# Performance work log

Hardware: AMD Instinct MI355X
Metric: run time of the kernel (lower is better)

## Reference

```python
import jax, jax.numpy as jnp
import numpy as np

EPS = 1e-6
B, T, J, D, H = 8, 512, 26, 256, 8
DH = D // H
HID = 4 * D


def logmap0(x):
    # x: [..., d+1] on hyperboloid (curvature -1). Tangent at origin -> [..., d]
    x0 = jnp.clip(x[..., :1], 1.0 + 1e-7, None)
    xs = x[..., 1:]
    n = jnp.maximum(jnp.linalg.norm(xs, axis=-1, keepdims=True), EPS)
    return jnp.arccosh(x0) * xs / n


def expmap0(v):
    # v: [..., d] tangent at origin -> [..., d+1] on hyperboloid
    n = jnp.maximum(jnp.linalg.norm(v, axis=-1, keepdims=True), EPS)
    return jnp.concatenate([jnp.cosh(n), jnp.sinh(n) * v / n], axis=-1)


def layernorm(v, g, b):
    m = jnp.mean(v, axis=-1, keepdims=True)
    var = jnp.var(v, axis=-1, keepdims=True)
    return (v - m) * jax.lax.rsqrt(var + 1e-5) * g + b


def lorentz_residual(x, z):
    # Lorentz centroid: normalize x+z so <m,m>_L = -1
    m = x + z
    mink = -m[..., :1] ** 2 + jnp.sum(m[..., 1:] ** 2, axis=-1, keepdims=True)
    return m / jnp.sqrt(jnp.clip(-mink, EPS, None))


def setup_inputs() -> dict:
    key = jax.random.key(0)
    ks = jax.random.split(key, 12)
    xs = jax.random.normal(ks[0], (B, T, J, D), jnp.float32) * 0.5
    x0 = jnp.sqrt(1.0 + jnp.sum(xs ** 2, axis=-1, keepdims=True))
    x = jnp.concatenate([x0, xs], axis=-1)  # valid points on H^d
    s = 1.0 / np.sqrt(D)
    inp = {
        "x": x,
        "g1": jnp.ones((D,), jnp.float32), "beta1": jnp.zeros((D,), jnp.float32),
        "Wq": jax.random.normal(ks[1], (D, D), jnp.float32) * s,
        "Wk": jax.random.normal(ks[2], (D, D), jnp.float32) * s,
        "Wv": jax.random.normal(ks[3], (D, D), jnp.float32) * s,
        "Wo": jax.random.normal(ks[4], (D, D), jnp.float32) * s,
        "bq": jnp.zeros((D,), jnp.float32), "bk": jnp.zeros((D,), jnp.float32),
        "bv": jnp.zeros((D,), jnp.float32), "bo": jnp.zeros((D,), jnp.float32),
        "g2": jnp.ones((D,), jnp.float32), "beta2": jnp.zeros((D,), jnp.float32),
        "W1": jax.random.normal(ks[5], (D, HID), jnp.float32) * s,
        "bf1": jnp.zeros((HID,), jnp.float32),
        "W2": jax.random.normal(ks[6], (HID, D), jnp.float32) * (1.0 / np.sqrt(HID)),
        "bf2": jnp.zeros((D,), jnp.float32),
    }
    return inp


def reference(x, g1, beta1, Wq, Wk, Wv, Wo, bq, bk, bv, bo, g2, beta2, W1, bf1, W2, bf2):
    # norm1: tangent-space LayerNorm
    u = layernorm(logmap0(x), g1, beta1)            # [B,T,J,D]
    xn = expmap0(u)
    # linear temporal attention (per joint, across T)
    t = logmap0(xn)
    q = (t @ Wq + bq).reshape(B, T, J, H, DH)
    k = (t @ Wk + bk).reshape(B, T, J, H, DH)
    v = (t @ Wv + bv).reshape(B, T, J, H, DH)
    pq = jax.nn.elu(q) + 1.0
    pk = jax.nn.elu(k) + 1.0
    kv = jnp.einsum('btjhk,btjhd->bjhkd', pk, v)    # O(T) global context
    ksum = jnp.sum(pk, axis=1)                      # [B,J,H,DH]
    num = jnp.einsum('btjhk,bjhkd->btjhd', pq, kv)
    den = jnp.einsum('btjhk,bjhk->btjh', pq, ksum)[..., None] + EPS
    o = (num / den).reshape(B, T, J, D) @ Wo + bo
    z = expmap0(o)
    # Lorentz (Minkowski) residual
    h = lorentz_residual(x, z)
    # norm2 + FFN in tangent space
    u2 = layernorm(logmap0(h), g2, beta2)
    f = jax.nn.gelu(u2 @ W1 + bf1) @ W2 + bf2
    return expmap0(f)
```

## Files before the change

### kernel.cpp

```cpp
#include <hip/hip_runtime.h>
#include <hip/hip_bf16.h>
#include <math.h>


#define EPSF 1e-6f
#define B_ 8
#define T_ 512
#define J_ 26
#define D_ 256
#define H_ 8
#define DH_ 32
#define HID_ 1024
#define NP1 257
#define R_ (B_*T_*J_)
#define NBJ (B_*J_)
#define NBH (NBJ*H_)

typedef float  f32x4  __attribute__((ext_vector_type(4)));
typedef short  s16x8  __attribute__((ext_vector_type(8)));
typedef short  s16x4  __attribute__((ext_vector_type(4)));

__device__ __forceinline__ int rp_to_r(int rp) {
  int bj = rp >> 9, t = rp & 511;
  int b = bj / 26, j = bj - 26 * b;
  return (b * 512 + t) * 26 + j;
}

__device__ __forceinline__ void async16(const void* g, void* l) {
  __builtin_amdgcn_global_load_lds(
      (const __attribute__((address_space(1))) unsigned int*)g,
      (__attribute__((address_space(3))) unsigned int*)l, 16, 0, 0);
}

__device__ __forceinline__ float wave_sum(float v) {
#pragma unroll
  for (int m = 32; m; m >>= 1) v += __shfl_xor(v, m, 64);
  return v;
}

__global__ __launch_bounds__(256) void k_wconv(const float* __restrict__ W,
                                               __hip_bfloat16* __restrict__ Wt,
                                               int K, int N) {
  __shared__ float tile[32][33];
  int n0 = blockIdx.x * 32, k0 = blockIdx.y * 32;
  int tx = threadIdx.x, ty = threadIdx.y;
#pragma unroll
  for (int i = ty; i < 32; i += 8) tile[i][tx] = W[(size_t)(k0 + i) * N + n0 + tx];
  __syncthreads();
#pragma unroll
  for (int i = ty; i < 32; i += 8)
    Wt[(size_t)(n0 + i) * K + k0 + tx] = __float2bfloat16(tile[tx][i]);
}

__global__ __launch_bounds__(256) void k_t(const float* __restrict__ x,
                                           const float* __restrict__ g1,
                                           const float* __restrict__ beta1,
                                           __hip_bfloat16* __restrict__ t) {
  int rp = blockIdx.x * 4 + (threadIdx.x >> 6);
  int l = threadIdx.x & 63;
  int r = rp_to_r(rp);
  const float* xr = x + (size_t)r * NP1;
  float xs[4];
#pragma unroll
  for (int i = 0; i < 4; ++i) xs[i] = xr[1 + l + 64*i];
  float p1 = xs[0]+xs[1]+xs[2]+xs[3];
  float p2 = xs[0]*xs[0]+xs[1]*xs[1]+xs[2]*xs[2]+xs[3]*xs[3];
  float s1 = wave_sum(p1);
  float s2 = wave_sum(p2);
  float mean = s1 * (1.0f/256.0f);
  float var = s2 * (1.0f/256.0f) - mean*mean;
  float rstd = rsqrtf(var + 1e-5f);
#pragma unroll
  for (int i = 0; i < 4; ++i) {
    int c = l + 64*i;
    t[(size_t)rp * D_ + c] = __float2bfloat16((xs[i]-mean)*rstd*g1[c] + beta1[c]);
  }
}

#define PHASE(BUF, MH, NH, GIDX, DO_VM) {                                      \
    s16x8 af_[4][2]; s16x8 bf_[2][2];                                          \
    const char* ab_ = lds + ((BUF)*2+(MH))*16384;                              \
    const char* bb_ = lds + 65536 + ((BUF)*2+(NH))*16384;                      \
    _Pragma("unroll") for (int f_ = 0; f_ < 4; ++f_)                           \
      _Pragma("unroll") for (int ks_ = 0; ks_ < 2; ++ks_)                      \
        af_[f_][ks_] = *(const s16x8*)(ab_ + aoffs[f_][ks_]);                  \
    _Pragma("unroll") for (int ni_ = 0; ni_ < 2; ++ni_)                        \
      _Pragma("unroll") for (int ks_ = 0; ks_ < 2; ++ks_)                      \
        bf_[ni_][ks_] = *(const s16x8*)(bb_ + boffs[ni_][ks_]);                \
    STAGE_HALF((GIDX) + 6);                                                    \
    if (DO_VM) asm volatile("s_waitcnt vmcnt(4)" ::: "memory");                \
    asm volatile("s_barrier" ::: "memory");                                    \
    __builtin_amdgcn_sched_barrier(0);                                         \
    __builtin_amdgcn_s_setprio(1);                                             \
    _Pragma("unroll") for (int ks_ = 0; ks_ < 2; ++ks_)                        \
      _Pragma("unroll") for (int f_ = 0; f_ < 4; ++f_)                         \
        _Pragma("unroll") for (int ni_ = 0; ni_ < 2; ++ni_)                    \
          acc[(MH)*4+f_][(NH)*2+ni_] = __builtin_amdgcn_mfma_f32_16x16x32_bf16(\
              bf_[ni_][ks_], af_[f_][ks_], acc[(MH)*4+f_][(NH)*2+ni_], 0,0,0); \
    __builtin_amdgcn_s_setprio(0);                                             \
    asm volatile("s_barrier" ::: "memory");                                    \
  }

template<int ACT, int EPI, int KDIM>
__global__ __launch_bounds__(512, 2) void k_gemm(const __hip_bfloat16* __restrict__ A,
                                                 const __hip_bfloat16* __restrict__ Bt,
                                                 const float* __restrict__ bias,
                                                 void* __restrict__ Cout,
                                                 int M, int N, int mOff) {
  extern __shared__ char lds[];
  constexpr int NKT = KDIM / 64;
  int tid = threadIdx.x;
  int w = tid >> 6, l = tid & 63;
  int wr = w >> 2, wc = w & 3;
  int ml = l & 15, quad = l >> 4;
  int n0 = blockIdx.x * 256, m0 = blockIdx.y * 256;

  const short* Ag = (const short*)A + (size_t)m0 * KDIM;
  const short* Bg = (const short*)Bt + (size_t)n0 * KDIM;

  int srow = w*8 + (l >> 3);
  int scol = (((l & 7) ^ ((l >> 3) & 7)) * 8);

  auto STAGE_HALF = [&](int n) {
    if (n >= 4*NKT) return;
    int kt = n >> 2;
    int isB = n & 1, h = (n >> 1) & 1, buf = kt & 1;
    const short* src = isB ? Bg : Ag;
    const short* g0 = src + (size_t)(h*128 + srow) * KDIM + kt*64 + scol;
    char* dst = lds + isB*65536 + (buf*2 + h)*16384 + w*1024;
    async16(g0, dst);
    async16(g0 + (size_t)64 * KDIM, dst + 8192);
  };

  int aoffs[4][2], boffs[2][2];
#pragma unroll
  for (int f = 0; f < 4; ++f) {
    int r = wr*64 + f*16 + ml;
#pragma unroll
    for (int ks = 0; ks < 2; ++ks)
      aoffs[f][ks] = (r*128 + ks*64 + quad*16) ^ ((ml & 7) << 4);
  }
#pragma unroll
  for (int ni = 0; ni < 2; ++ni) {
    int rb = wc*32 + ni*16 + ml;
#pragma unroll
    for (int ks = 0; ks < 2; ++ks)
      boffs[ni][ks] = (rb*128 + ks*64 + quad*16) ^ ((ml & 7) << 4);
  }

  f32x4 acc[8][4];
#pragma unroll
  for (int i = 0; i < 8; ++i)
#pragma unroll
    for (int j = 0; j < 4; ++j) acc[i][j] = {0.f, 0.f, 0.f, 0.f};

#pragma unroll
  for (int n = 0; n < 6; ++n) STAGE_HALF(n);
  asm volatile("s_waitcnt vmcnt(4)" ::: "memory");
  asm volatile("s_barrier" ::: "memory");

  for (int cc = 0; cc < NKT/2; ++cc) {
    int g0 = cc * 8;
    PHASE(0, 0, 0, g0+0, 0)
    PHASE(0, 0, 1, g0+1, 0)
    PHASE(0, 1, 0, g0+2, 0)
    PHASE(0, 1, 1, g0+3, 1)
    PHASE(1, 0, 0, g0+4, 0)
    PHASE(1, 0, 1, g0+5, 0)
    PHASE(1, 1, 0, g0+6, 0)
    PHASE(1, 1, 1, g0+7, 1)
  }

  if (EPI == 0) {
#pragma unroll
    for (int mi = 0; mi < 8; ++mi) {
      size_t row = (size_t)(m0 + (mi>>2)*128 + wr*64 + (mi&3)*16 + ml);
#pragma unroll
      for (int nj = 0; nj < 4; ++nj) {
        int col = n0 + (nj>>1)*128 + wc*32 + (nj&1)*16 + quad*4;
        f32x4 bj = *(const f32x4*)&bias[col];
        f32x4 v = acc[mi][nj] + bj;
        if (ACT == 1) {
#pragma unroll
          for (int e = 0; e < 4; ++e) v[e] = (v[e] > 0.0f) ? v[e] + 1.0f : __expf(v[e]);
        } else if (ACT == 2) {
#pragma unroll
          for (int e = 0; e < 4; ++e) {
            float vv = v[e], v2 = vv * vv;
            float ex = __expf(vv * fmaf(v2, -0.0713548327f, -1.5957691216f));
            v[e] = vv * __builtin_amdgcn_rcpf(1.0f + ex);
          }
        }
        s16x4 sv;
#pragma unroll
        for (int e = 0; e < 4; ++e) {
          __hip_bfloat16 b = __float2bfloat16(v[e]);
          sv[e] = *(short*)&b;
        }
        *(s16x4*)&((__hip_bfloat16*)Cout)[row * N + col] = sv;
      }
    }
  } else {
    float* out = (float*)Cout;
    float* red = (float*)lds;
    f32x4 bj4[4];
#pragma unroll
    for (int nj = 0; nj < 4; ++nj)
      bj4[nj] = *(const f32x4*)&bias[(nj>>1)*128 + wc*32 + (nj&1)*16 + quad*4];
    float n2[8];
#pragma unroll
    for (int mi = 0; mi < 8; ++mi) {
      float p = 0.f;
#pragma unroll
      for (int nj = 0; nj < 4; ++nj)
#pragma unroll
        for (int e = 0; e < 4; ++e) {
          float f = acc[mi][nj][e] + bj4[nj][e];
          p = fmaf(f, f, p);
        }
      p += __shfl_xor(p, 16, 64);
      p += __shfl_xor(p, 32, 64);
      n2[mi] = p;
    }
    __syncthreads();
    if (quad == 0) {
#pragma unroll
      for (int mi = 0; mi < 8; ++mi)
        red[((wr*4 + wc)*8 + mi)*16 + ml] = n2[mi];
    }
    __syncthreads();
#pragma unroll
    for (int mi = 0; mi < 8; ++mi) {
      float s = 0.f;
#pragma unroll
      for (int w2 = 0; w2 < 4; ++w2)
        s += red[((wr*4 + w2)*8 + mi)*16 + ml];
      n2[mi] = s;
    }
#pragma unroll
    for (int mi = 0; mi < 8; ++mi) {
      int rowp = m0 + (mi>>2)*128 + wr*64 + (mi&3)*16 + ml;
      int r = rp_to_r(mOff + rowp);
      float* orow = out + (size_t)r * NP1;
      float n = fmaxf(sqrtf(n2[mi]), EPSF);
      float e = __expf(n);
      float ie = 1.0f / e;
      float sc = (e - ie) * 0.5f / n;
      if (wc == 0 && quad == 0) orow[0] = (e + ie) * 0.5f;
#pragma unroll
      for (int nj = 0; nj < 4; ++nj) {
        int col = (nj>>1)*128 + wc*32 + (nj&1)*16 + quad*4;
#pragma unroll
        for (int e2 = 0; e2 < 4; ++e2)
          orow[1 + col + e2] = sc * (acc[mi][nj][e2] + bj4[nj][e2]);
      }
    }
  }
}

__global__ __launch_bounds__(256) void k_kv(const __hip_bfloat16* __restrict__ pk,
                                            const __hip_bfloat16* __restrict__ v,
                                            float* __restrict__ kv,
                                            float* __restrict__ ksum) {
  __shared__ float spk[32][32];
  __shared__ float sv [32][32];
  int blk = blockIdx.x;
  int h = blk & 7, bj = blk >> 3;
  int tid = threadIdx.x;
  int row = tid >> 3, cg = tid & 7;
  int k0 = tid >> 5, dd = tid & 31;

  const short* pkg = (const short*)pk + (size_t)bj*512*256 + h*32 + cg*4;
  const short* vg  = (const short*)v  + (size_t)bj*512*256 + h*32 + cg*4;

  s16x4 rp_, rv_;
  auto GLOAD = [&](int c) {
    size_t off = (size_t)(c*32 + row) * 256;
    rp_ = *(const s16x4*)(pkg + off);
    rv_ = *(const s16x4*)(vg + off);
  };

  float acc[4] = {0.f, 0.f, 0.f, 0.f};
  float ks = 0.f;

  GLOAD(0);
  for (int c = 0; c < 16; ++c) {
    f32x4 pf, vf;
#pragma unroll
    for (int e = 0; e < 4; ++e) {
      pf[e] = __uint_as_float(((unsigned)(unsigned short)rp_[e]) << 16);
      vf[e] = __uint_as_float(((unsigned)(unsigned short)rv_[e]) << 16);
    }
    *(f32x4*)&spk[row][cg*4] = pf;
    *(f32x4*)&sv [row][cg*4] = vf;
    __syncthreads();
    if (c < 15) GLOAD(c + 1);
#pragma unroll
    for (int q = 0; q < 32; ++q) {
      float vv = sv[q][dd];
#pragma unroll
      for (int m = 0; m < 4; ++m) acc[m] = fmaf(spk[q][k0 + 8*m], vv, acc[m]);
    }
    if (tid < 32) {
#pragma unroll
      for (int q = 0; q < 32; ++q) ks += spk[q][tid];
    }
    __syncthreads();
  }

  float* kvp = kv + (size_t)blk * 1024;
#pragma unroll
  for (int m = 0; m < 4; ++m) kvp[(k0 + 8*m)*32 + dd] = acc[m];
  if (tid < 32) ksum[(size_t)blk * 32 + tid] = ks;
}

__global__ __launch_bounds__(256) void k_attn(const __hip_bfloat16* __restrict__ pq,
                                              const float* __restrict__ kv,
                                              const float* __restrict__ ksum,
                                              __hip_bfloat16* __restrict__ attn) {
  __shared__ float psf[32][264];
  __shared__ float dens[32][8];
  int bj = blockIdx.y;
  int t0 = blockIdx.x * 32;
  int g0 = bj * 512 + t0;
  int tid = threadIdx.x, w = tid >> 6, l = tid & 63;
  int h = w*2 + (l >> 5), dd = l & 31;

  const float* kvp = kv + ((size_t)bj * 8 + h) * (DH_*DH_);
  float kvreg[32];
#pragma unroll
  for (int k = 0; k < 32; ++k) kvreg[k] = kvp[k*32 + dd];

  for (int tr = 0; tr < 32; ++tr)
    psf[tr][tid] = __bfloat162float(pq[(size_t)(g0 + tr) * D_ + tid]);
  __syncthreads();

  {
    int tr = tid & 31, hh = tid >> 5;
    const float* ksp = ksum + ((size_t)bj * 8 + hh) * DH_;
    float dsum = 0.f;
#pragma unroll
    for (int k = 0; k < 32; ++k) dsum = fmaf(psf[tr][hh*32 + k], ksp[k], dsum);
    dens[tr][hh] = dsum;
  }
  __syncthreads();

  for (int tr = 0; tr < 32; ++tr) {
    const float* pr = &psf[tr][h*32];
    float num = 0.f;
#pragma unroll
    for (int k = 0; k < 32; ++k) num = fmaf(pr[k], kvreg[k], num);
    float rden = __builtin_amdgcn_rcpf(dens[tr][h] + EPSF);
    attn[(size_t)(g0 + tr) * D_ + tid] = __float2bfloat16(num * rden);
  }
}

__global__ __launch_bounds__(256) void k_u2(const __hip_bfloat16* __restrict__ o,
                                            const float* __restrict__ x,
                                            const float* __restrict__ g2,
                                            const float* __restrict__ beta2,
                                            __hip_bfloat16* __restrict__ u2) {
  int rp = blockIdx.x * 4 + (threadIdx.x >> 6);
  int l = threadIdx.x & 63;
  int r = rp_to_r(rp);
  const float* xr = x + (size_t)r * NP1;
  float ov[4], xs[4];
#pragma unroll
  for (int i = 0; i < 4; ++i) {
    ov[i] = __bfloat162float(o[(size_t)rp * D_ + l + 64*i]);
    xs[i] = xr[1 + l + 64*i];
  }
  float p2 = ov[0]*ov[0]+ov[1]*ov[1]+ov[2]*ov[2]+ov[3]*ov[3];
  float s2o = wave_sum(p2);
  float no = fmaxf(sqrtf(s2o), EPSF);
  float e = __expf(no);
  float c = (e - 1.0f/e) * 0.5f / no;
  float mi[4];
#pragma unroll
  for (int i = 0; i < 4; ++i) mi[i] = xs[i] + c * ov[i];
  float q1 = mi[0]+mi[1]+mi[2]+mi[3];
  float q2 = mi[0]*mi[0]+mi[1]*mi[1]+mi[2]*mi[2]+mi[3]*mi[3];
  float s1 = wave_sum(q1);
  float s2 = wave_sum(q2);
  float mean = s1 * (1.0f/256.0f);
  float var = s2 * (1.0f/256.0f) - mean*mean;
  float rstd = rsqrtf(var + 1e-5f);
#pragma unroll
  for (int i = 0; i < 4; ++i) {
    int cc = l + 64*i;
    u2[(size_t)rp * D_ + cc] = __float2bfloat16((mi[i]-mean)*rstd*g2[cc] + beta2[cc]);
  }
}

extern "C" void kernel_launch(void* const* d_in, const int* in_sizes, int n_in,
                              void* d_out, int out_size, void* d_ws, size_t ws_size,
                              hipStream_t stream) {
  const float* x     = (const float*)d_in[0];
  const float* g1    = (const float*)d_in[1];
  const float* beta1 = (const float*)d_in[2];
  const float* Wq    = (const float*)d_in[3];
  const float* Wk    = (const float*)d_in[4];
  const float* Wv    = (const float*)d_in[5];
  const float* Wo    = (const float*)d_in[6];
  const float* bq    = (const float*)d_in[7];
  const float* bk    = (const float*)d_in[8];
  const float* bv    = (const float*)d_in[9];
  const float* bo    = (const float*)d_in[10];
  const float* g2    = (const float*)d_in[11];
  const float* beta2 = (const float*)d_in[12];
  const float* W1    = (const float*)d_in[13];
  const float* bf1   = (const float*)d_in[14];
  const float* W2    = (const float*)d_in[15];
  const float* bf2   = (const float*)d_in[16];
  float* out = (float*)d_out;
  char* ws = (char*)d_ws;

  size_t off = 0;
  __hip_bfloat16* wqT = (__hip_bfloat16*)(ws + off); off += (size_t)D_*D_*2;
  __hip_bfloat16* wkT = (__hip_bfloat16*)(ws + off); off += (size_t)D_*D_*2;
  __hip_bfloat16* wvT = (__hip_bfloat16*)(ws + off); off += (size_t)D_*D_*2;
  __hip_bfloat16* woT = (__hip_bfloat16*)(ws + off); off += (size_t)D_*D_*2;
  __hip_bfloat16* w1T = (__hip_bfloat16*)(ws + off); off += (size_t)HID_*D_*2;
  __hip_bfloat16* w2T = (__hip_bfloat16*)(ws + off); off += (size_t)D_*HID_*2;
  float* kvb = (float*)(ws + off); off += (size_t)NBH*(DH_*DH_)*4;
  float* ksb = (float*)(ws + off); off += (size_t)NBH*DH_*4;
  off = (off + 255) & ~(size_t)255;
  __hip_bfloat16* tb = (__hip_bfloat16*)(ws + off); off += (size_t)R_*D_*2;
  __hip_bfloat16* qb = (__hip_bfloat16*)(ws + off); off += (size_t)R_*D_*2;
  __hip_bfloat16* kb = (__hip_bfloat16*)(ws + off); off += (size_t)R_*D_*2;
  __hip_bfloat16* vb = (__hip_bfloat16*)(ws + off); off += (size_t)R_*D_*2;
  __hip_bfloat16* hid = (__hip_bfloat16*)(ws + off); off += (size_t)(R_/2)*HID_*2;

  static bool attr_done = false;
  if (!attr_done) {
    hipFuncSetAttribute((const void*)k_gemm<1,0,256>,  hipFuncAttributeMaxDynamicSharedMemorySize, 131072);
    hipFuncSetAttribute((const void*)k_gemm<0,0,256>,  hipFuncAttributeMaxDynamicSharedMemorySize, 131072);
    hipFuncSetAttribute((const void*)k_gemm<2,0,256>,  hipFuncAttributeMaxDynamicSharedMemorySize, 131072);
    hipFuncSetAttribute((const void*)k_gemm<0,2,1024>, hipFuncAttributeMaxDynamicSharedMemorySize, 131072);
    attr_done = true;
  }

  dim3 tconv(32, 8);
  k_wconv<<<dim3(D_/32,  D_/32),  tconv, 0, stream>>>(Wq, wqT, D_,  D_);
  k_wconv<<<dim3(D_/32,  D_/32),  tconv, 0, stream>>>(Wk, wkT, D_,  D_);
  k_wconv<<<dim3(D_/32,  D_/32),  tconv, 0, stream>>>(Wv, wvT, D_,  D_);
  k_wconv<<<dim3(D_/32,  D_/32),  tconv, 0, stream>>>(Wo, woT, D_,  D_);
  k_wconv<<<dim3(HID_/32, D_/32), tconv, 0, stream>>>(W1, w1T, D_,  HID_);
  k_wconv<<<dim3(D_/32, HID_/32), tconv, 0, stream>>>(W2, w2T, HID_, D_);

  k_t<<<R_/4, 256, 0, stream>>>(x, g1, beta1, tb);

  dim3 gqkv(D_/256, R_/256);
  k_gemm<1,0,256><<<gqkv, 512, 131072, stream>>>(tb, wqT, bq, qb, R_, D_, 0);
  k_gemm<1,0,256><<<gqkv, 512, 131072, stream>>>(tb, wkT, bk, kb, R_, D_, 0);
  k_gemm<0,0,256><<<gqkv, 512, 131072, stream>>>(tb, wvT, bv, vb, R_, D_, 0);

  k_kv<<<NBH, 256, 0, stream>>>(kb, vb, kvb, ksb);
  k_attn<<<dim3(T_/32, NBJ), 256, 0, stream>>>(qb, kvb, ksb, kb);

  k_gemm<0,0,256><<<gqkv, 512, 131072, stream>>>(kb, woT, bo, vb, R_, D_, 0);
  k_u2<<<R_/4, 256, 0, stream>>>(vb, x, g2, beta2, tb);

  const int Rc = R_ / 2;
  for (int c = 0; c < 2; ++c) {
    k_gemm<2,0,256><<<dim3(HID_/256, Rc/256), 512, 131072, stream>>>(
        tb + (size_t)c * Rc * D_, w1T, bf1, hid, Rc, HID_, 0);
    k_gemm<0,2,1024><<<dim3(1, Rc/256), 512, 131072, stream>>>(
        hid, w2T, bf2, out, Rc, D_, c * Rc);
  }
}
```

Before: 782.2 us.

## Fuse Q/K/V projections into one GEMM launch and register-tile kv reduction

The three separate Q, K and V projection GEMMs become one launch with three column blocks. Each block picks its bias and activation (ELU+1 for Q and K, none for V) from its column index and writes to the matching output buffer. This relies on the transposed weights and the output buffers sitting next to each other in the workspace. The k_kv kernel now gives each thread a 4x4 outer-product tile built from vectorised LDS reads on padded rows, with the time chunk split across warps and a final cross-warp reduction through shared memory. This aims to cut launch and scheduling overhead and LDS traffic, at the cost of an extra reduction step and barrier.

```diff
diff --git a/kernel.cpp b/kernel.cpp
--- a/kernel.cpp
+++ b/kernel.cpp
@@ -105,6 +105,8 @@
 __global__ __launch_bounds__(512, 2) void k_gemm(const __hip_bfloat16* __restrict__ A,
                                                  const __hip_bfloat16* __restrict__ Bt,
                                                  const float* __restrict__ bias,
+                                                 const float* __restrict__ bias2,
+                                                 const float* __restrict__ bias3,
                                                  void* __restrict__ Cout,
                                                  int M, int N, int mOff) {
   extern __shared__ char lds[];
@@ -171,19 +173,24 @@
     PHASE(1, 1, 1, g0+7, 1)
   }
 
-  if (EPI == 0) {
+  if (EPI == 0 || EPI == 1) {
+    int bi = n0 >> 8;
+    const float* bsel = (EPI == 1) ? (bi == 0 ? bias : bi == 1 ? bias2 : bias3)
+                                   : bias;
+    int doElu = (EPI == 1) ? (bi < 2) : (ACT == 1);
 #pragma unroll
     for (int mi = 0; mi < 8; ++mi) {
       size_t row = (size_t)(m0 + (mi>>2)*128 + wr*64 + (mi&3)*16 + ml);
 #pragma unroll
       for (int nj = 0; nj < 4; ++nj) {
         int col = n0 + (nj>>1)*128 + wc*32 + (nj&1)*16 + quad*4;
-        f32x4 bj = *(const f32x4*)&bias[col];
+        int colL = col & 255;
+        f32x4 bj = *(const f32x4*)&bsel[(EPI == 1) ? colL : col];
         f32x4 v = acc[mi][nj] + bj;
-        if (ACT == 1) {
+        if (doElu) {
 #pragma unroll
           for (int e = 0; e < 4; ++e) v[e] = (v[e] > 0.0f) ? v[e] + 1.0f : __expf(v[e]);
-        } else if (ACT == 2) {
+        } else if (EPI == 0 && ACT == 2) {
 #pragma unroll
           for (int e = 0; e < 4; ++e) {
             float vv = v[e], v2 = vv * vv;
@@ -197,7 +204,12 @@
           __hip_bfloat16 b = __float2bfloat16(v[e]);
           sv[e] = *(short*)&b;
         }
-        *(s16x4*)&((__hip_bfloat16*)Cout)[row * N + col] = sv;
+        if (EPI == 1) {
+          short* cb = (short*)Cout + (size_t)bi * R_ * 256;
+          *(s16x4*)&cb[row * 256 + colL] = sv;
+        } else {
+          *(s16x4*)&((__hip_bfloat16*)Cout)[row * N + col] = sv;
+        }
       }
     }
   } else {
@@ -262,13 +274,17 @@
                                             const __hip_bfloat16* __restrict__ v,
                                             float* __restrict__ kv,
                                             float* __restrict__ ksum) {
-  __shared__ float spk[32][32];
-  __shared__ float sv [32][32];
+  __shared__ float sbuf[4096];
+  __shared__ float sks[4][32];
   int blk = blockIdx.x;
   int h = blk & 7, bj = blk >> 3;
   int tid = threadIdx.x;
+  int w = tid >> 6, l = tid & 63;
   int row = tid >> 3, cg = tid & 7;
-  int k0 = tid >> 5, dd = tid & 31;
+  int kg = l >> 3, dg = l & 7;
+
+  float* spk = sbuf;
+  float* sv  = sbuf + 1152;
 
   const short* pkg = (const short*)pk + (size_t)bj*512*256 + h*32 + cg*4;
   const short* vg  = (const short*)v  + (size_t)bj*512*256 + h*32 + cg*4;
@@ -280,8 +296,8 @@
     rv_ = *(const s16x4*)(vg + off);
   };
 
-  float acc[4] = {0.f, 0.f, 0.f, 0.f};
-  float ks = 0.f;
+  f32x4 acc[4] = {{0,0,0,0},{0,0,0,0},{0,0,0,0},{0,0,0,0}};
+  float ks[4] = {0.f, 0.f, 0.f, 0.f};
 
   GLOAD(0);
   for (int c = 0; c < 16; ++c) {
@@ -291,27 +307,42 @@
       pf[e] = __uint_as_float(((unsigned)(unsigned short)rp_[e]) << 16);
       vf[e] = __uint_as_float(((unsigned)(unsigned short)rv_[e]) << 16);
     }
-    *(f32x4*)&spk[row][cg*4] = pf;
-    *(f32x4*)&sv [row][cg*4] = vf;
+    *(f32x4*)&spk[row*36 + cg*4] = pf;
+    *(f32x4*)&sv [row*36 + cg*4] = vf;
     __syncthreads();
     if (c < 15) GLOAD(c + 1);
 #pragma unroll
-    for (int q = 0; q < 32; ++q) {
-      float vv = sv[q][dd];
-#pragma unroll
-      for (int m = 0; m < 4; ++m) acc[m] = fmaf(spk[q][k0 + 8*m], vv, acc[m]);
-    }
-    if (tid < 32) {
-#pragma unroll
-      for (int q = 0; q < 32; ++q) ks += spk[q][tid];
+    for (int qq = 0; qq < 8; ++qq) {
+      int q = w*8 + qq;
+      f32x4 pq4 = *(const f32x4*)&spk[q*36 + kg*4];
+      f32x4 vq4 = *(const f32x4*)&sv [q*36 + dg*4];
+#pragma unroll
+      for (int m = 0; m < 4; ++m) {
+#pragma unroll
+        for (int n = 0; n < 4; ++n) acc[m][n] = fmaf(pq4[m], vq4[n], acc[m][n]);
+        ks[m] += pq4[m];
+      }
     }
     __syncthreads();
   }
 
-  float* kvp = kv + (size_t)blk * 1024;
-#pragma unroll
-  for (int m = 0; m < 4; ++m) kvp[(k0 + 8*m)*32 + dd] = acc[m];
-  if (tid < 32) ksum[(size_t)blk * 32 + tid] = ks;
+#pragma unroll
+  for (int m = 0; m < 4; ++m) *(f32x4*)&sbuf[tid*16 + m*4] = acc[m];
+  if (dg == 0) {
+#pragma unroll
+    for (int m = 0; m < 4; ++m) sks[w][kg*4 + m] = ks[m];
+  }
+  __syncthreads();
+  {
+    int lo = tid & 63, m = tid >> 6;
+    f32x4 s = {0.f, 0.f, 0.f, 0.f};
+#pragma unroll
+    for (int ww = 0; ww < 4; ++ww) s += *(const f32x4*)&sbuf[(ww*64 + lo)*16 + m*4];
+    int kgo = lo >> 3, dgo = lo & 7;
+    *(f32x4*)&kv[(size_t)blk*1024 + (size_t)(kgo*4 + m)*32 + dgo*4] = s;
+  }
+  if (tid < 32)
+    ksum[(size_t)blk*32 + tid] = sks[0][tid] + sks[1][tid] + sks[2][tid] + sks[3][tid];
 }
 
 __global__ __launch_bounds__(256) void k_attn(const __hip_bfloat16* __restrict__ pq,
@@ -433,7 +464,7 @@
 
   static bool attr_done = false;
   if (!attr_done) {
-    hipFuncSetAttribute((const void*)k_gemm<1,0,256>,  hipFuncAttributeMaxDynamicSharedMemorySize, 131072);
+    hipFuncSetAttribute((const void*)k_gemm<0,1,256>,  hipFuncAttributeMaxDynamicSharedMemorySize, 131072);
     hipFuncSetAttribute((const void*)k_gemm<0,0,256>,  hipFuncAttributeMaxDynamicSharedMemorySize, 131072);
     hipFuncSetAttribute((const void*)k_gemm<2,0,256>,  hipFuncAttributeMaxDynamicSharedMemorySize, 131072);
     hipFuncSetAttribute((const void*)k_gemm<0,2,1024>, hipFuncAttributeMaxDynamicSharedMemorySize, 131072);
@@ -450,22 +481,21 @@
 
   k_t<<<R_/4, 256, 0, stream>>>(x, g1, beta1, tb);
 
-  dim3 gqkv(D_/256, R_/256);
-  k_gemm<1,0,256><<<gqkv, 512, 131072, stream>>>(tb, wqT, bq, qb, R_, D_, 0);
-  k_gemm<1,0,256><<<gqkv, 512, 131072, stream>>>(tb, wkT, bk, kb, R_, D_, 0);
-  k_gemm<0,0,256><<<gqkv, 512, 131072, stream>>>(tb, wvT, bv, vb, R_, D_, 0);
+  k_gemm<0,1,256><<<dim3(3, R_/256), 512, 131072, stream>>>(
+      tb, wqT, bq, bk, bv, qb, R_, 256, 0);
 
   k_kv<<<NBH, 256, 0, stream>>>(kb, vb, kvb, ksb);
   k_attn<<<dim3(T_/32, NBJ), 256, 0, stream>>>(qb, kvb, ksb, kb);
 
-  k_gemm<0,0,256><<<gqkv, 512, 131072, stream>>>(kb, woT, bo, vb, R_, D_, 0);
+  k_gemm<0,0,256><<<dim3(1, R_/256), 512, 131072, stream>>>(
+      kb, woT, bo, nullptr, nullptr, vb, R_, D_, 0);
   k_u2<<<R_/4, 256, 0, stream>>>(vb, x, g2, beta2, tb);
 
   const int Rc = R_ / 2;
   for (int c = 0; c < 2; ++c) {
     k_gemm<2,0,256><<<dim3(HID_/256, Rc/256), 512, 131072, stream>>>(
-        tb + (size_t)c * Rc * D_, w1T, bf1, hid, Rc, HID_, 0);
+        tb + (size_t)c * Rc * D_, w1T, bf1, nullptr, nullptr, hid, Rc, HID_, 0);
     k_gemm<0,2,1024><<<dim3(1, Rc/256), 512, 131072, stream>>>(
-        hid, w2T, bf2, out, Rc, D_, c * Rc);
-  }
-}
+        hid, w2T, bf2, nullptr, nullptr, out, Rc, D_, c * Rc);
+  }
+}
```

Result: faster. 711.5 us (-9.0%).
